# Kernel tuning notes

Hardware: AMD Instinct MI355X
Metric: run time of the kernel (lower is better)

Reference implementation:

```python
import jax, jax.numpy as jnp
import numpy as np

N = 50000      # nodes
E = 800000     # edges
G = 512        # graphs in batch
F0 = 92        # orig atom feature len
F = 64         # atom_fea_len
NB = 41        # nbr_fea_len
H = 128        # h_fea_len
NCONV = 3
EPS = 1e-5


def setup_inputs() -> dict:
    key = jax.random.key(0)
    ks = jax.random.split(key, 16)
    s = 0.05
    inp = {
        "x": jax.random.normal(ks[0], (N, F0), jnp.float32),
        "edge_index": jax.random.randint(ks[1], (2, E), 0, N),
        "edge_attr": jax.random.normal(ks[2], (E, NB), jnp.float32),
        "batch": jnp.sort(jax.random.randint(ks[3], (N,), 0, G)),
        # embedding (only applied at the first conv, when x width == F0)
        "emb_W": jax.random.normal(ks[4], (F0, F), jnp.float32) * s,
        "emb_b": jnp.zeros((F,), jnp.float32),
        # per-conv-layer params, stacked on leading axis
        "bn1_g": jnp.ones((NCONV, F), jnp.float32),
        "bn1_b": jnp.zeros((NCONV, F), jnp.float32),
        "bn2_g": jnp.ones((NCONV, F), jnp.float32),
        "bn2_b": jnp.zeros((NCONV, F), jnp.float32),
        "lnf_W": jax.random.normal(ks[5], (NCONV, 2 * F + NB, F), jnp.float32) * s,
        "lnf_b": jnp.zeros((NCONV, F), jnp.float32),
        "lns_W": jax.random.normal(ks[6], (NCONV, 2 * F + NB, F), jnp.float32) * s,
        "lns_b": jnp.zeros((NCONV, F), jnp.float32),
        # readout MLP
        "fc1_W": jax.random.normal(ks[7], (F, H), jnp.float32) * s,
        "fc1_b": jnp.zeros((H,), jnp.float32),
        "out_W": jax.random.normal(ks[8], (H, 1), jnp.float32) * s,
        "out_b": jnp.zeros((1,), jnp.float32),
    }
    return inp


def _batchnorm(x, g, b):
    # training-mode BatchNorm1d: batch stats over node dim, biased variance
    mean = jnp.mean(x, axis=0)
    var = jnp.var(x, axis=0)
    return (x - mean) * jax.lax.rsqrt(var + EPS) * g + b


def _cgconv(x, edge_index, edge_attr, bn1_g, bn1_b, bn2_g, bn2_b, Wf, bf, Ws, bs):
    x = _batchnorm(x, bn1_g, bn1_b)
    # flow='target_to_source': x_i = x[edge_index[0]], x_j = x[edge_index[1]],
    # aggregation scatter-adds messages to edge_index[0]
    src, dst = edge_index[0], edge_index[1]
    z = jnp.concatenate([x[src], x[dst], edge_attr], axis=-1)   # [E, 2F+NB]
    m = jax.nn.sigmoid(z @ Wf + bf) * jax.nn.softplus(z @ Ws + bs)
    agg = jax.ops.segment_sum(m, src, num_segments=x.shape[0])  # [N, F]
    out = _batchnorm(agg, bn2_g, bn2_b) + x
    return jax.nn.softplus(out)


def reference(x, edge_index, edge_attr, batch, emb_W, emb_b,
              bn1_g, bn1_b, bn2_g, bn2_b, lnf_W, lnf_b, lns_W, lns_b,
              fc1_W, fc1_b, out_W, out_b):
    h = x @ emb_W + emb_b  # first conv applies embedding (x width == F0)
    for i in range(NCONV):
        h = _cgconv(h, edge_index, edge_attr,
                    bn1_g[i], bn1_b[i], bn2_g[i], bn2_b[i],
                    lnf_W[i], lnf_b[i], lns_W[i], lns_b[i])
    # global mean pool per graph
    sums = jax.ops.segment_sum(h, batch, num_segments=G)
    cnts = jax.ops.segment_sum(jnp.ones((h.shape[0], 1), h.dtype), batch, num_segments=G)
    crys = sums / jnp.maximum(cnts, 1.0)                         # [G, F]
    crys = jax.nn.softplus(jax.nn.softplus(crys) @ fc1_W + fc1_b)
    return crys @ out_W + out_b                                  # [G, 1]
```

## Files before the change

kernel.cpp:

```cpp
#include <hip/hip_runtime.h>

#define NN 50000
#define NE 800000
#define NG 512
#define F0 92
#define FF 64
#define NB 41
#define HH 128

typedef float f4 __attribute__((ext_vector_type(4)));
typedef float f4u __attribute__((ext_vector_type(4), aligned(4)));

__device__ __forceinline__ float softplusf(float x) {
    return fmaxf(x, 0.f) + __logf(1.f + __expf(-fabsf(x)));
}
__device__ __forceinline__ float sigmoidf(float x) {
    return __fdividef(1.f, 1.f + __expf(-x));
}

__global__ __launch_bounds__(256, 4) void emb_kernel(
    const float* __restrict__ x, const float* __restrict__ W,
    const float* __restrict__ bias, float* __restrict__ h)
{
    __shared__ float sx[4][F0];
    const int lane = threadIdx.x & 63;
    const int w = threadIdx.x >> 6;
    float wr[F0];
#pragma unroll
    for (int k = 0; k < F0; ++k) wr[k] = W[k * FF + lane];
    const float bv = bias[lane];
    const int nit = NN / 4;
    for (int it = blockIdx.x; it < nit; it += gridDim.x) {
        const int n = it * 4 + w;
        if (lane < 46) {
            sx[w][lane * 2]     = x[n * F0 + lane * 2];
            sx[w][lane * 2 + 1] = x[n * F0 + lane * 2 + 1];
        }
        __syncthreads();
        float acc = bv;
#pragma unroll
        for (int k4 = 0; k4 < F0 / 4; ++k4) {
            float4 q = *(const float4*)&sx[w][k4 * 4];
            acc = fmaf(q.x, wr[k4 * 4 + 0], acc);
            acc = fmaf(q.y, wr[k4 * 4 + 1], acc);
            acc = fmaf(q.z, wr[k4 * 4 + 2], acc);
            acc = fmaf(q.w, wr[k4 * 4 + 3], acc);
        }
        h[n * FF + lane] = acc;
        __syncthreads();
    }
}

__global__ __launch_bounds__(256) void stats_kernel(
    const float* __restrict__ src, float* __restrict__ stats)
{
    __shared__ float sd[2][4][FF];
    const int f = threadIdx.x & 63;
    const int r = threadIdx.x >> 6;
    float s = 0.f, s2 = 0.f;
    for (int n = blockIdx.x * 4 + r; n < NN; n += gridDim.x * 4) {
        float v = src[n * FF + f];
        s += v;
        s2 = fmaf(v, v, s2);
    }
    sd[0][r][f] = s;
    sd[1][r][f] = s2;
    __syncthreads();
    if (threadIdx.x < FF) {
        float ts = sd[0][0][f] + sd[0][1][f] + sd[0][2][f] + sd[0][3][f];
        float t2 = sd[1][0][f] + sd[1][1][f] + sd[1][2][f] + sd[1][3][f];
        atomicAdd(&stats[f], ts);
        atomicAdd(&stats[FF + f], t2);
    }
}

__global__ void finalize_kernel(const float* __restrict__ g, const float* __restrict__ b,
                                float* __restrict__ stats)
{
    const int f = threadIdx.x;
    const float inv = 1.f / (float)NN;
    float mean = stats[f] * inv;
    float var = stats[FF + f] * inv - mean * mean;
    float rstd = rsqrtf(var + 1e-5f);
    float A = rstd * g[f];
    stats[2 * FF + f] = A;
    stats[3 * FF + f] = fmaf(-mean, A, b[f]);
}

__global__ __launch_bounds__(256) void prep_kernel(
    const float* __restrict__ lnfW, const float* __restrict__ lnsW,
    float* __restrict__ wTe)
{
    const int total = 3 * 2 * 64 * 44;
    for (int idx = blockIdx.x * 256 + threadIdx.x; idx < total; idx += gridDim.x * 256) {
        const int k = idx % 44;
        const int lane = (idx / 44) & 63;
        const int m = (idx / (44 * 64)) & 1;
        const int i = idx / (44 * 64 * 2);
        const float* W = (m == 0 ? lnfW : lnsW) + (size_t)i * 169 * FF;
        wTe[idx] = (k < NB) ? W[(2 * FF + k) * FF + lane] : 0.f;
    }
}

__global__ __launch_bounds__(256, 4) void node_kernel(
    const float* __restrict__ h, const float* __restrict__ stats,
    const float* __restrict__ Wf, const float* __restrict__ Ws,
    const float* __restrict__ bf, const float* __restrict__ bs,
    float* __restrict__ xn, float* __restrict__ pS, float* __restrict__ pD)
{
    __shared__ float sx[4][FF];
    const int lane = threadIdx.x & 63;
    const int w = threadIdx.x >> 6;
    const float* W = (w < 2) ? Wf : Ws;
    const int rowbase = (w & 1) * FF;
    float wr[FF];
#pragma unroll
    for (int k = 0; k < FF; ++k) wr[k] = W[(rowbase + k) * FF + lane];
    const float A = stats[2 * FF + lane];
    const float B = stats[3 * FF + lane];
    float bias = 0.f;
    if (w == 0) bias = bf[lane];
    if (w == 2) bias = bs[lane];
    float* outp = ((w & 1) ? pD : pS) + ((w >> 1) & 1);
    for (int n = blockIdx.x; n < NN; n += gridDim.x) {
        const float xv = fmaf(h[n * FF + lane], A, B);
        if (w == 0) xn[n * FF + lane] = xv;
        sx[w][lane] = xv;
        __syncthreads();
        float acc = bias;
#pragma unroll
        for (int k4 = 0; k4 < FF / 4; ++k4) {
            float4 q = *(const float4*)&sx[w][k4 * 4];
            acc = fmaf(q.x, wr[k4 * 4 + 0], acc);
            acc = fmaf(q.y, wr[k4 * 4 + 1], acc);
            acc = fmaf(q.z, wr[k4 * 4 + 2], acc);
            acc = fmaf(q.w, wr[k4 * 4 + 3], acc);
        }
        outp[(size_t)n * 128 + 2 * lane] = acc;
        __syncthreads();
    }
}

__global__ __launch_bounds__(256) __attribute__((amdgpu_waves_per_eu(4, 4)))
void edge_kernel(
    const int* __restrict__ ei, const float* __restrict__ ea,
    const float* __restrict__ wTe,
    const float* __restrict__ pS, const float* __restrict__ pD,
    float* __restrict__ agg)
{
    const int lane = threadIdx.x & 63;
    const int w = threadIdx.x >> 6;
    const float* wtf = wTe + (size_t)lane * 44;
    const float* wts = wTe + (size_t)(FF + lane) * 44;
    f4 wfr[11], wsr[11];
#pragma unroll
    for (int k4 = 0; k4 < 11; ++k4) {
        wfr[k4] = *(const f4*)&wtf[k4 * 4];
        wsr[k4] = *(const f4*)&wts[k4 * 4];
    }
    const int nit = NE / 4;
    for (int it = blockIdx.x; it < nit; it += gridDim.x) {
        const int e = __builtin_amdgcn_readfirstlane(it * 4 + w);
        const int src = ei[e];
        const int dst = ei[NE + e];
        const float2 gS = *(const float2*)(pS + (size_t)src * 128 + 2 * lane);
        const float2 gD = *(const float2*)(pD + (size_t)dst * 128 + 2 * lane);
        const float* er = ea + (size_t)e * NB;
        float accF = 0.f, accS = 0.f;
#pragma unroll
        for (int k4 = 0; k4 < 10; ++k4) {
            const f4u q = *(const f4u*)(er + k4 * 4);
            accF = fmaf(q.x, wfr[k4].x, accF); accS = fmaf(q.x, wsr[k4].x, accS);
            accF = fmaf(q.y, wfr[k4].y, accF); accS = fmaf(q.y, wsr[k4].y, accS);
            accF = fmaf(q.z, wfr[k4].z, accF); accS = fmaf(q.z, wsr[k4].z, accS);
            accF = fmaf(q.w, wfr[k4].w, accF); accS = fmaf(q.w, wsr[k4].w, accS);
        }
        const float q40 = er[40];
        accF = fmaf(q40, wfr[10].x, accF);
        accS = fmaf(q40, wsr[10].x, accS);
        accF += gS.x + gD.x;
        accS += gS.y + gD.y;
        const float m = sigmoidf(accF) * softplusf(accS);
        unsafeAtomicAdd(&agg[(size_t)src * FF + lane], m);
    }
}

__global__ __launch_bounds__(256) void update_kernel(
    const float* __restrict__ agg, const float* __restrict__ xn,
    const float* __restrict__ stats, float* __restrict__ h,
    const int* __restrict__ batch, float* __restrict__ pool,
    float* __restrict__ pcnt, const int do_pool)
{
    const int total = NN * FF;
    for (int idx = blockIdx.x * blockDim.x + threadIdx.x; idx < total;
         idx += gridDim.x * blockDim.x) {
        const int f = idx & 63;
        const int n = idx >> 6;
        const float A = stats[2 * FF + f];
        const float B = stats[3 * FF + f];
        const float v = softplusf(fmaf(agg[idx], A, B) + xn[idx]);
        if (do_pool) {
            const int g = batch[n];
            unsafeAtomicAdd(&pool[g * FF + f], v);
            if (f == 0) unsafeAtomicAdd(&pcnt[g], 1.f);
        } else {
            h[idx] = v;
        }
    }
}

__global__ __launch_bounds__(128) void readout_kernel(
    const float* __restrict__ pool, const float* __restrict__ pcnt,
    const float* __restrict__ fc1W, const float* __restrict__ fc1b,
    const float* __restrict__ outW, const float* __restrict__ outb,
    float* __restrict__ out)
{
    __shared__ float sp[FF];
    __shared__ float red[2];
    const int g = blockIdx.x;
    const int t = threadIdx.x;
    if (t < FF) {
        const float c = fmaxf(pcnt[g], 1.f);
        sp[t] = softplusf(pool[g * FF + t] / c);
    }
    __syncthreads();
    float a = fc1b[t];
#pragma unroll
    for (int k = 0; k < FF; ++k) a = fmaf(sp[k], fc1W[k * HH + t], a);
    float o = softplusf(a) * outW[t];
#pragma unroll
    for (int off = 32; off > 0; off >>= 1) o += __shfl_down(o, off, 64);
    if ((t & 63) == 0) red[t >> 6] = o;
    __syncthreads();
    if (t == 0) out[g] = red[0] + red[1] + outb[0];
}

extern "C" void kernel_launch(void* const* d_in, const int* in_sizes, int n_in,
                              void* d_out, int out_size, void* d_ws, size_t ws_size,
                              hipStream_t stream)
{
    const float* x     = (const float*)d_in[0];
    const int*   ei    = (const int*)  d_in[1];
    const float* ea    = (const float*)d_in[2];
    const int*   batch = (const int*)  d_in[3];
    const float* embW  = (const float*)d_in[4];
    const float* embb  = (const float*)d_in[5];
    const float* bn1g  = (const float*)d_in[6];
    const float* bn1b  = (const float*)d_in[7];
    const float* bn2g  = (const float*)d_in[8];
    const float* bn2b  = (const float*)d_in[9];
    const float* lnfW  = (const float*)d_in[10];
    const float* lnfb  = (const float*)d_in[11];
    const float* lnsW  = (const float*)d_in[12];
    const float* lnsb  = (const float*)d_in[13];
    const float* fc1W  = (const float*)d_in[14];
    const float* fc1b  = (const float*)d_in[15];
    const float* outW  = (const float*)d_in[16];
    const float* outb  = (const float*)d_in[17];

    float* ws    = (float*)d_ws;
    float* h     = ws;
    float* xn    = h    + (size_t)NN * FF;
    float* pS    = xn   + (size_t)NN * FF;
    float* pD    = pS   + (size_t)NN * 128;
    float* agg   = pD   + (size_t)NN * 128;
    float* stats = agg  + (size_t)NN * FF;
    float* pool  = stats + 4 * FF;
    float* pcnt  = pool + (size_t)NG * FF;
    float* wTe   = pcnt + NG;

    hipMemsetAsync(pool, 0, (NG * FF + NG) * sizeof(float), stream);
    prep_kernel<<<66, 256, 0, stream>>>(lnfW, lnsW, wTe);
    emb_kernel<<<1024, 256, 0, stream>>>(x, embW, embb, h);

    for (int i = 0; i < 3; ++i) {
        const float* Wf  = lnfW + (size_t)i * 169 * FF;
        const float* Wsp = lnsW + (size_t)i * 169 * FF;
        hipMemsetAsync(stats, 0, 2 * FF * sizeof(float), stream);
        stats_kernel<<<256, 256, 0, stream>>>(h, stats);
        finalize_kernel<<<1, 64, 0, stream>>>(bn1g + i * FF, bn1b + i * FF, stats);
        node_kernel<<<1024, 256, 0, stream>>>(h, stats, Wf, Wsp,
                                              lnfb + i * FF, lnsb + i * FF, xn, pS, pD);
        hipMemsetAsync(agg, 0, (size_t)NN * FF * sizeof(float), stream);
        edge_kernel<<<2048, 256, 0, stream>>>(ei, ea, wTe + (size_t)i * 2 * FF * 44,
                                              pS, pD, agg);
        hipMemsetAsync(stats, 0, 2 * FF * sizeof(float), stream);
        stats_kernel<<<256, 256, 0, stream>>>(agg, stats);
        finalize_kernel<<<1, 64, 0, stream>>>(bn2g + i * FF, bn2b + i * FF, stats);
        update_kernel<<<2048, 256, 0, stream>>>(agg, xn, stats, h, batch, pool, pcnt,
                                                (i == 2) ? 1 : 0);
    }
    readout_kernel<<<NG, HH, 0, stream>>>(pool, pcnt, fc1W, fc1b, outW, outb, (float*)d_out);
}
```

Before: 1.073 ms.

## Build CSR by source node once and aggregate edges per node without atomics

Adds a one-time histogram, three-pass prefix scan and scatter that sort edges by source into CSR form (edge id plus destination). The edge kernel then gives one wave per source node, loops over its edges, accumulates the message in a register and writes agg once. This removes the float atomics and the per-layer memset of agg, and reuses pS across a node's edges. In exchange it adds preprocessing kernels, makes edge_attr reads indirect and non-sequential, and can leave waves unevenly loaded when node degrees vary. It also splits the FMA chains into two accumulators and drops the occupancy hint on node_kernel.

```diff
diff --git a/kernel.cpp b/kernel.cpp
--- a/kernel.cpp
+++ b/kernel.cpp
@@ -7,6 +7,7 @@
 #define FF 64
 #define NB 41
 #define HH 128
+#define NBLK_SCAN 196
 
 typedef float f4 __attribute__((ext_vector_type(4)));
 typedef float f4u __attribute__((ext_vector_type(4), aligned(4)));
@@ -18,7 +19,84 @@
     return __fdividef(1.f, 1.f + __expf(-x));
 }
 
-__global__ __launch_bounds__(256, 4) void emb_kernel(
+
+__global__ __launch_bounds__(256) void hist_kernel(const int* __restrict__ ei,
+                                                   int* __restrict__ cnt)
+{
+    for (int e = blockIdx.x * 256 + threadIdx.x; e < NE; e += gridDim.x * 256)
+        atomicAdd(&cnt[ei[e]], 1);
+}
+
+__global__ __launch_bounds__(256) void scan1_kernel(const int* __restrict__ cnt,
+                                                    int* __restrict__ bsum)
+{
+    __shared__ int sd[256];
+    const int t = threadIdx.x;
+    const int idx = blockIdx.x * 256 + t;
+    sd[t] = (idx < NN) ? cnt[idx] : 0;
+    __syncthreads();
+    for (int s = 128; s > 0; s >>= 1) {
+        if (t < s) sd[t] += sd[t + s];
+        __syncthreads();
+    }
+    if (t == 0) bsum[blockIdx.x] = sd[0];
+}
+
+__global__ __launch_bounds__(256) void scan2_kernel(int* __restrict__ bsum,
+                                                    int* __restrict__ rowptr)
+{
+    __shared__ int sd[256];
+    const int t = threadIdx.x;
+    const int v = (t < NBLK_SCAN) ? bsum[t] : 0;
+    sd[t] = v;
+    __syncthreads();
+    for (int off = 1; off < 256; off <<= 1) {
+        int a = (t >= off) ? sd[t - off] : 0;
+        __syncthreads();
+        sd[t] += a;
+        __syncthreads();
+    }
+    if (t < NBLK_SCAN) bsum[t] = sd[t] - v;
+    if (t == 255) rowptr[NN] = sd[255];
+}
+
+__global__ __launch_bounds__(256) void scan3_kernel(const int* __restrict__ cnt,
+                                                    const int* __restrict__ bsum,
+                                                    int* __restrict__ rowptr,
+                                                    int* __restrict__ cursor)
+{
+    __shared__ int sd[256];
+    const int t = threadIdx.x;
+    const int idx = blockIdx.x * 256 + t;
+    const int v = (idx < NN) ? cnt[idx] : 0;
+    sd[t] = v;
+    __syncthreads();
+    for (int off = 1; off < 256; off <<= 1) {
+        int a = (t >= off) ? sd[t - off] : 0;
+        __syncthreads();
+        sd[t] += a;
+        __syncthreads();
+    }
+    if (idx < NN) {
+        const int ex = bsum[blockIdx.x] + sd[t] - v;
+        rowptr[idx] = ex;
+        cursor[idx] = ex;
+    }
+}
+
+__global__ __launch_bounds__(256) void scatter_kernel(const int* __restrict__ ei,
+                                                      int* __restrict__ cursor,
+                                                      int2* __restrict__ sorted)
+{
+    for (int e = blockIdx.x * 256 + threadIdx.x; e < NE; e += gridDim.x * 256) {
+        const int s = ei[e];
+        const int pos = atomicAdd(&cursor[s], 1);
+        sorted[pos] = make_int2(e, ei[NE + e]);
+    }
+}
+
+
+__global__ __launch_bounds__(256) void emb_kernel(
     const float* __restrict__ x, const float* __restrict__ W,
     const float* __restrict__ bias, float* __restrict__ h)
 {
@@ -102,7 +180,7 @@
     }
 }
 
-__global__ __launch_bounds__(256, 4) void node_kernel(
+__global__ __launch_bounds__(256) void node_kernel(
     const float* __restrict__ h, const float* __restrict__ stats,
     const float* __restrict__ Wf, const float* __restrict__ Ws,
     const float* __restrict__ bf, const float* __restrict__ bs,
@@ -143,13 +221,12 @@
 
 __global__ __launch_bounds__(256) __attribute__((amdgpu_waves_per_eu(4, 4)))
 void edge_kernel(
-    const int* __restrict__ ei, const float* __restrict__ ea,
-    const float* __restrict__ wTe,
+    const int2* __restrict__ sorted, const float* __restrict__ ea,
+    const int* __restrict__ rowptr, const float* __restrict__ wTe,
     const float* __restrict__ pS, const float* __restrict__ pD,
     float* __restrict__ agg)
 {
     const int lane = threadIdx.x & 63;
-    const int w = threadIdx.x >> 6;
     const float* wtf = wTe + (size_t)lane * 44;
     const float* wts = wTe + (size_t)(FF + lane) * 44;
     f4 wfr[11], wsr[11];
@@ -157,31 +234,42 @@
     for (int k4 = 0; k4 < 11; ++k4) {
         wfr[k4] = *(const f4*)&wtf[k4 * 4];
         wsr[k4] = *(const f4*)&wts[k4 * 4];
-    }
-    const int nit = NE / 4;
-    for (int it = blockIdx.x; it < nit; it += gridDim.x) {
-        const int e = __builtin_amdgcn_readfirstlane(it * 4 + w);
-        const int src = ei[e];
-        const int dst = ei[NE + e];
-        const float2 gS = *(const float2*)(pS + (size_t)src * 128 + 2 * lane);
-        const float2 gD = *(const float2*)(pD + (size_t)dst * 128 + 2 * lane);
-        const float* er = ea + (size_t)e * NB;
-        float accF = 0.f, accS = 0.f;
-#pragma unroll
-        for (int k4 = 0; k4 < 10; ++k4) {
-            const f4u q = *(const f4u*)(er + k4 * 4);
-            accF = fmaf(q.x, wfr[k4].x, accF); accS = fmaf(q.x, wsr[k4].x, accS);
-            accF = fmaf(q.y, wfr[k4].y, accF); accS = fmaf(q.y, wsr[k4].y, accS);
-            accF = fmaf(q.z, wfr[k4].z, accF); accS = fmaf(q.z, wsr[k4].z, accS);
-            accF = fmaf(q.w, wfr[k4].w, accF); accS = fmaf(q.w, wsr[k4].w, accS);
-        }
-        const float q40 = er[40];
-        accF = fmaf(q40, wfr[10].x, accF);
-        accS = fmaf(q40, wsr[10].x, accS);
-        accF += gS.x + gD.x;
-        accS += gS.y + gD.y;
-        const float m = sigmoidf(accF) * softplusf(accS);
-        unsafeAtomicAdd(&agg[(size_t)src * FF + lane], m);
+        asm volatile("" : "+v"(wfr[k4]), "+v"(wsr[k4]));
+    }
+    const int nwave = (gridDim.x * blockDim.x) >> 6;
+    const int wid = (blockIdx.x * blockDim.x + threadIdx.x) >> 6;
+    for (int n0 = wid; n0 < NN; n0 += nwave) {
+        const int n = __builtin_amdgcn_readfirstlane(n0);
+        const int rs = rowptr[n];
+        const int re = rowptr[n + 1];
+        const float2 gS = *(const float2*)(pS + (size_t)n * 128 + 2 * lane);
+        float acc = 0.f;
+        for (int e = rs; e < re; ++e) {
+            const int2 sd2 = sorted[e];
+            const int se = sd2.x;
+            const int dst = sd2.y;
+            const float2 gD = *(const float2*)(pD + (size_t)dst * 128 + 2 * lane);
+            const float* er = ea + (size_t)se * NB;
+            float aF0 = gS.x, aF1 = gD.x, aS0 = gS.y, aS1 = gD.y;
+#pragma unroll
+            for (int k4 = 0; k4 < 10; k4 += 2) {
+                const f4u q0 = *(const f4u*)(er + k4 * 4);
+                const f4u q1 = *(const f4u*)(er + k4 * 4 + 4);
+                aF0 = fmaf(q0.x, wfr[k4].x, aF0);     aS0 = fmaf(q0.x, wsr[k4].x, aS0);
+                aF0 = fmaf(q0.y, wfr[k4].y, aF0);     aS0 = fmaf(q0.y, wsr[k4].y, aS0);
+                aF0 = fmaf(q0.z, wfr[k4].z, aF0);     aS0 = fmaf(q0.z, wsr[k4].z, aS0);
+                aF0 = fmaf(q0.w, wfr[k4].w, aF0);     aS0 = fmaf(q0.w, wsr[k4].w, aS0);
+                aF1 = fmaf(q1.x, wfr[k4 + 1].x, aF1); aS1 = fmaf(q1.x, wsr[k4 + 1].x, aS1);
+                aF1 = fmaf(q1.y, wfr[k4 + 1].y, aF1); aS1 = fmaf(q1.y, wsr[k4 + 1].y, aS1);
+                aF1 = fmaf(q1.z, wfr[k4 + 1].z, aF1); aS1 = fmaf(q1.z, wsr[k4 + 1].z, aS1);
+                aF1 = fmaf(q1.w, wfr[k4 + 1].w, aF1); aS1 = fmaf(q1.w, wsr[k4 + 1].w, aS1);
+            }
+            const float q40 = er[40];
+            aF0 = fmaf(q40, wfr[10].x, aF0);
+            aS0 = fmaf(q40, wsr[10].x, aS0);
+            acc += sigmoidf(aF0 + aF1) * softplusf(aS0 + aS1);
+        }
+        agg[(size_t)n * FF + lane] = acc;
     }
 }
 
@@ -268,6 +356,18 @@
     float* pool  = stats + 4 * FF;
     float* pcnt  = pool + (size_t)NG * FF;
     float* wTe   = pcnt + NG;
+    int*   cnt    = (int*)(wTe + 3 * 2 * 64 * 44);
+    int*   rowptr = cnt + NN;
+    int*   cursor = rowptr + NN + 2;
+    int*   bsum   = cursor + NN;
+    int2*  sorted = (int2*)(bsum + 256);
+
+    hipMemsetAsync(cnt, 0, NN * sizeof(int), stream);
+    hist_kernel<<<2048, 256, 0, stream>>>(ei, cnt);
+    scan1_kernel<<<NBLK_SCAN, 256, 0, stream>>>(cnt, bsum);
+    scan2_kernel<<<1, 256, 0, stream>>>(bsum, rowptr);
+    scan3_kernel<<<NBLK_SCAN, 256, 0, stream>>>(cnt, bsum, rowptr, cursor);
+    scatter_kernel<<<2048, 256, 0, stream>>>(ei, cursor, sorted);
 
     hipMemsetAsync(pool, 0, (NG * FF + NG) * sizeof(float), stream);
     prep_kernel<<<66, 256, 0, stream>>>(lnfW, lnsW, wTe);
@@ -281,9 +381,8 @@
         finalize_kernel<<<1, 64, 0, stream>>>(bn1g + i * FF, bn1b + i * FF, stats);
         node_kernel<<<1024, 256, 0, stream>>>(h, stats, Wf, Wsp,
                                               lnfb + i * FF, lnsb + i * FF, xn, pS, pD);
-        hipMemsetAsync(agg, 0, (size_t)NN * FF * sizeof(float), stream);
-        edge_kernel<<<2048, 256, 0, stream>>>(ei, ea, wTe + (size_t)i * 2 * FF * 44,
-                                              pS, pD, agg);
+        edge_kernel<<<1024, 256, 0, stream>>>(sorted, ea, rowptr,
+                                              wTe + (size_t)i * 2 * FF * 44, pS, pD, agg);
         hipMemsetAsync(stats, 0, 2 * FF * sizeof(float), stream);
         stats_kernel<<<256, 256, 0, stream>>>(agg, stats);
         finalize_kernel<<<1, 64, 0, stream>>>(bn2g + i * FF, bn2b + i * FF, stats);
```

Result: no change. 1.083 ms (+0.9%).
